# Kernel tuning notes

Hardware: AMD Instinct MI355X
Metric: run time of the kernel (lower is better)

The kernel has to match this reference:

```python
import jax, jax.numpy as jnp
import numpy as np

B = 32; IMG = 224; P = 16; D = 768; NH = 12; HD = 64; L = 12; MLP = 3072; S0 = 197
NE = 10; LP = 40; NPL = 5; NC = 100; EPS = 1e-6
POS_PROMPT = (0, 1, 2, 3, 4)


def setup_inputs() -> dict:
    ks = jax.random.split(jax.random.key(0), 18)
    n = lambda k, shp: jax.random.normal(k, shp, jnp.float32) * 0.02
    return {
        "inputs": jax.random.normal(ks[0], (B, 3, IMG, IMG), jnp.float32),
        "expert_ids": jax.random.randint(ks[1], (B,), 0, NE),
        "patch_w": n(ks[2], (D, 3, P, P)),
        "patch_b": n(ks[3], (D,)),
        "cls_token": n(ks[4], (1, 1, D)),
        "pos_embed": n(ks[5], (1, S0, D)),
        "ln1_s": jnp.ones((L, D), jnp.float32),
        "ln1_b": jnp.zeros((L, D), jnp.float32),
        "qkv_w": n(ks[6], (L, D, 3 * D)),
        "qkv_b": n(ks[7], (L, 3 * D)),
        "proj_w": n(ks[8], (L, D, D)),
        "proj_b": n(ks[9], (L, D)),
        "ln2_s": jnp.ones((L, D), jnp.float32),
        "ln2_b": jnp.zeros((L, D), jnp.float32),
        "fc1_w": n(ks[10], (L, D, MLP)),
        "fc1_b": n(ks[11], (L, MLP)),
        "fc2_w": n(ks[12], (L, MLP, D)),
        "fc2_b": n(ks[13], (L, D)),
        "norm_s": jnp.ones((D,), jnp.float32),
        "norm_b": jnp.zeros((D,), jnp.float32),
        "prompts": jax.random.uniform(ks[14], (NPL, NE, LP, D), jnp.float32),
        "head_w": n(ks[15], (NE, D, NC)),
        "head_b": n(ks[16], (NE, NC)),
    }


def _ln(x, s, b):
    m = x.mean(-1, keepdims=True)
    v = ((x - m) ** 2).mean(-1, keepdims=True)
    return (x - m) * jax.lax.rsqrt(v + EPS) * s + b


def _forward(inputs, expert_ids, patch_w, patch_b, cls_token, pos_embed,
             ln1_s, ln1_b, qkv_w, qkv_b, proj_w, proj_b, ln2_s, ln2_b,
             fc1_w, fc1_b, fc2_w, fc2_b, norm_s, norm_b, prompts, head_w, head_b):
    # patch embed: conv stride 16 -> [B, D, 14, 14] -> [B, 196, D]
    x = jax.lax.conv_general_dilated(inputs, patch_w, (P, P), 'VALID',
                                     dimension_numbers=('NCHW', 'OIHW', 'NCHW'))
    x = x.reshape(B, D, -1).transpose(0, 2, 1) + patch_b
    x = jnp.concatenate([jnp.broadcast_to(cls_token, (B, 1, D)), x], axis=1) + pos_embed
    # per-sample expert prompt gather: [B, NPL, LP, D], plus cls pos bias
    bp = jnp.take(prompts, expert_ids, axis=1).transpose(1, 0, 2, 3) + pos_embed[0, 0]
    scale = 1.0 / np.sqrt(HD)
    for i in range(L):
        if i in POS_PROMPT:
            x = jnp.concatenate([x, bp[:, POS_PROMPT.index(i)]], axis=1)
        S = x.shape[1]
        h = _ln(x, ln1_s[i], ln1_b[i])
        qkv = (h @ qkv_w[i] + qkv_b[i]).reshape(B, S, 3, NH, HD).transpose(2, 0, 3, 1, 4)
        q, k, v = qkv[0], qkv[1], qkv[2]
        att = jax.nn.softmax(jnp.einsum('bhqd,bhkd->bhqk', q, k) * scale, axis=-1)
        o = jnp.einsum('bhqk,bhkd->bhqd', att, v).transpose(0, 2, 1, 3).reshape(B, S, D)
        x = x + o @ proj_w[i] + proj_b[i]
        h = _ln(x, ln2_s[i], ln2_b[i])
        x = x + jax.nn.gelu(h @ fc1_w[i] + fc1_b[i], approximate=False) @ fc2_w[i] + fc2_b[i]
        x = x[:, :S0]  # drop prompt tokens after each block
    feat = _ln(x, norm_s, norm_b)[:, 0]
    # per-sample expert head dispatch: gathered-weight batched matvec
    return jnp.einsum('bd,bdc->bc', feat, head_w[expert_ids]) + head_b[expert_ids]


def reference(inputs, expert_ids, patch_w, patch_b, cls_token, pos_embed,
              ln1_s, ln1_b, qkv_w, qkv_b, proj_w, proj_b, ln2_s, ln2_b,
              fc1_w, fc1_b, fc2_w, fc2_b, norm_s, norm_b, prompts, head_w, head_b):
    return _forward(inputs, expert_ids, patch_w, patch_b, cls_token, pos_embed,
                    ln1_s, ln1_b, qkv_w, qkv_b, proj_w, proj_b, ln2_s, ln2_b,
                    fc1_w, fc1_b, fc2_w, fc2_b, norm_s, norm_b, prompts, head_w, head_b)
```

## Files before the change

kernel.cpp:

```cpp
#include <hip/hip_runtime.h>

typedef unsigned short ushort_t;
typedef __attribute__((ext_vector_type(8))) short short8;
typedef __attribute__((ext_vector_type(4))) short shortx4;
typedef __attribute__((ext_vector_type(4))) float floatx4;

#define D_    768
#define SMAX  237
#define S0_   197
#define RPAD  7680
#define NHEAD 12
#define BATCH 32


__device__ __forceinline__ ushort_t f2bf(float f) {
  union { float f; unsigned u; } v; v.f = f;
  unsigned r = v.u + 0x7FFFu + ((v.u >> 16) & 1u);
  return (ushort_t)(r >> 16);
}
__device__ __forceinline__ float bf2f(ushort_t u) {
  union { unsigned u; float f; } v; v.u = ((unsigned)u) << 16; return v.f;
}
__device__ __forceinline__ void async16(const void* g, void* l) {
  __builtin_amdgcn_global_load_lds((const __attribute__((address_space(1))) void*)g,
                                   (__attribute__((address_space(3))) void*)l, 16, 0, 0);
}

__global__ __launch_bounds__(256) void patchify_kernel(
    const float* __restrict__ in, ushort_t* __restrict__ Xp) {
  int rowid = blockIdx.x;
  int b = rowid / 196, p = rowid - b * 196;
  int py = p / 14, px = p - py * 14;
  int tid = threadIdx.x;
#pragma unroll
  for (int t = 0; t < 3; ++t) {
    int k = tid + t * 256;
    int c = k >> 8, rem = k & 255, i = rem >> 4, j = rem & 15;
    float v = in[(((size_t)b * 3 + c) * 224 + py * 16 + i) * 224 + px * 16 + j];
    Xp[(size_t)rowid * 768 + k] = f2bf(v);
  }
}

__global__ void cvt_bf16_kernel(const float* __restrict__ src, ushort_t* __restrict__ dst, int n) {
  int i = blockIdx.x * 256 + threadIdx.x;
  if (i < n) dst[i] = f2bf(src[i]);
}

__global__ void cls_fill_kernel(const float* __restrict__ cls, const float* __restrict__ pos,
                                float* __restrict__ X) {
  int b = blockIdx.x, d = threadIdx.x;
  X[(size_t)b * 768 + d] = cls[d] + pos[d];
}

__global__ void prompt_fill_kernel(const float* __restrict__ prompts, const float* __restrict__ pos,
                                   const int* __restrict__ eid, float* __restrict__ X, int layer) {
  int id = blockIdx.x;
  int b = id / 40, p = id - b * 40;
  int e = eid[b];
  float v = prompts[(((size_t)layer * 10 + e) * 40 + p) * 768 + threadIdx.x] + pos[threadIdx.x];
  X[((size_t)(197 + p) * 32 + b) * 768 + threadIdx.x] = v;
}

__global__ __launch_bounds__(256) void transpose_wts_kernel(
    const float* __restrict__ qkvw, const float* __restrict__ projw,
    const float* __restrict__ fc1w, const float* __restrict__ fc2w,
    ushort_t* __restrict__ wq, ushort_t* __restrict__ wp,
    ushort_t* __restrict__ w1, ushort_t* __restrict__ w2,
    int l0, int slot_mul) {
  int id = blockIdx.x;
  int l = l0 + id / 1728;
  int t = id % 1728;
  size_t s = (size_t)(l * slot_mul);
  const float* src; ushort_t* dst; int K, N;
  if (t < 432)       { src = qkvw + (size_t)l * 768 * 2304; dst = wq + s * 2304 * 768; K = 768;  N = 2304; }
  else if (t < 576)  { src = projw + (size_t)l * 768 * 768;  dst = wp + s * 768 * 768;  K = 768;  N = 768;  t -= 432; }
  else if (t < 1152) { src = fc1w + (size_t)l * 768 * 3072;  dst = w1 + s * 768 * 3072; K = 768;  N = 3072; t -= 576; }
  else               { src = fc2w + (size_t)l * 3072 * 768;  dst = w2 + s * 3072 * 768; K = 3072; N = 768;  t -= 1152; }
  int ntn = N >> 6;
  int k0 = (t / ntn) * 64, n0 = (t % ntn) * 64;
  __shared__ float tile[64][65];
  int tid = threadIdx.x;
#pragma unroll
  for (int q = 0; q < 4; ++q) {
    int slot = q * 256 + tid;
    int r = slot >> 4, c4 = (slot & 15) * 4;
    floatx4 v = *(const floatx4*)&src[(size_t)(k0 + r) * N + n0 + c4];
    tile[r][c4] = v[0]; tile[r][c4 + 1] = v[1]; tile[r][c4 + 2] = v[2]; tile[r][c4 + 3] = v[3];
  }
  __syncthreads();
#pragma unroll
  for (int q = 0; q < 2; ++q) {
    int slot = q * 256 + tid;
    int n = slot >> 3, kc = (slot & 7) * 8;
    short8 o;
#pragma unroll
    for (int e = 0; e < 8; ++e) o[e] = (short)f2bf(tile[kc + e][n]);
    *(short8*)&dst[(size_t)(n0 + n) * K + k0 + kc] = o;
  }
}

__global__ __launch_bounds__(256) void ln_kernel(
    const float* __restrict__ X, const float* __restrict__ s, const float* __restrict__ bt,
    ushort_t* __restrict__ H) {
  int row = blockIdx.x * 4 + (threadIdx.x >> 6);
  int lane = threadIdx.x & 63;
  const float* xr = X + (size_t)row * 768;
  floatx4 v0 = *(const floatx4*)&xr[lane * 4];
  floatx4 v1 = *(const floatx4*)&xr[256 + lane * 4];
  floatx4 v2 = *(const floatx4*)&xr[512 + lane * 4];
  float sum = 0.f, sq = 0.f;
#pragma unroll
  for (int e = 0; e < 4; ++e) {
    sum += v0[e] + v1[e] + v2[e];
    sq  += v0[e] * v0[e] + v1[e] * v1[e] + v2[e] * v2[e];
  }
#pragma unroll
  for (int m = 1; m <= 32; m <<= 1) {
    sum += __shfl_xor(sum, m, 64);
    sq  += __shfl_xor(sq,  m, 64);
  }
  float mean = sum * (1.f / 768.f);
  float var  = sq * (1.f / 768.f) - mean * mean;
  float rs = rsqrtf(var + 1e-6f);
  ushort_t* hr = H + (size_t)row * 768;
#pragma unroll
  for (int w = 0; w < 3; ++w) {
    const floatx4 v = (w == 0) ? v0 : (w == 1) ? v1 : v2;
    shortx4 o;
#pragma unroll
    for (int e = 0; e < 4; ++e) {
      int d = w * 256 + lane * 4 + e;
      o[e] = (short)f2bf((v[e] - mean) * rs * s[d] + bt[d]);
    }
    *(shortx4*)&hr[w * 256 + lane * 4] = o;
  }
}

enum { EPI_BF16 = 0, EPI_GELU = 1, EPI_RESID = 2, EPI_PATCH = 3 };

template <int EPI>
__device__ __forceinline__ void epi_store(float accv, int row, int col,
                                          const float* bias, float* XO, ushort_t* O,
                                          const float* pos, int N) {
  if (EPI == EPI_BF16) {
    O[(size_t)row * N + col] = f2bf(accv + bias[col]);
  } else if (EPI == EPI_GELU) {
    float v = accv + bias[col];
    float g = 0.5f * v * (1.0f + erff(v * 0.70710678118f));
    O[(size_t)row * N + col] = f2bf(g);
  } else if (EPI == EPI_RESID) {
    XO[(size_t)row * 768 + col] += accv + bias[col];
  } else {
    int b = row / 196, p = row - b * 196;
    size_t orow = (size_t)(1 + p) * 32 + b;
    XO[orow * 768 + col] = accv + bias[col] + pos[(size_t)(1 + p) * 768 + col];
  }
}

template <int EPI>
__global__ __launch_bounds__(256) void gemm_kernel(
    const ushort_t* __restrict__ A, int lda,
    const ushort_t* __restrict__ BT,
    const float* __restrict__ bias,
    float* __restrict__ XO, ushort_t* __restrict__ O,
    const float* __restrict__ pos,
    int N, int K) {
  __shared__ ushort_t As[128 * 64];
  __shared__ ushort_t Bs[128 * 64];
  int m0 = blockIdx.y * 128, n0 = blockIdx.x * 128;
  int tid = threadIdx.x, lane = tid & 63, wv = tid >> 6;
  int wm = (wv >> 1) * 64, wn = (wv & 1) * 64;
  int fr = lane & 15, kg = lane >> 4;
  int sw = (fr >> 1) & 7;

  floatx4 acc[4][4];
#pragma unroll
  for (int i = 0; i < 4; ++i)
#pragma unroll
    for (int j = 0; j < 4; ++j) acc[i][j] = (floatx4){0.f, 0.f, 0.f, 0.f};

  for (int k0 = 0; k0 < K; k0 += 64) {
#pragma unroll
    for (int t = 0; t < 4; ++t) {
      int flat = (wv * 4 + t) * 64 + lane;
      int row = flat >> 3;
      int ch = ((flat & 7) ^ ((row >> 1) & 7)) * 8;
      async16(A + (size_t)(m0 + row) * lda + k0 + ch, &As[(wv * 4 + t) * 512]);
      async16(BT + (size_t)(n0 + row) * K + k0 + ch, &Bs[(wv * 4 + t) * 512]);
    }
    __syncthreads();
#pragma unroll
    for (int kh = 0; kh < 2; ++kh) {
      short8 af[4], bfr[4];
#pragma unroll
      for (int i = 0; i < 4; ++i)
        af[i] = *(const short8*)&As[(wm + i * 16 + fr) * 64 + (((kh * 4 + kg) ^ sw) * 8)];
#pragma unroll
      for (int j = 0; j < 4; ++j)
        bfr[j] = *(const short8*)&Bs[(wn + j * 16 + fr) * 64 + (((kh * 4 + kg) ^ sw) * 8)];
#pragma unroll
      for (int i = 0; i < 4; ++i)
#pragma unroll
        for (int j = 0; j < 4; ++j)
          acc[i][j] = __builtin_amdgcn_mfma_f32_16x16x32_bf16(af[i], bfr[j], acc[i][j], 0, 0, 0);
    }
    __syncthreads();
  }

  int rbase = (lane >> 4) * 4;
#pragma unroll
  for (int i = 0; i < 4; ++i)
#pragma unroll
    for (int j = 0; j < 4; ++j) {
      int col = n0 + wn + j * 16 + fr;
#pragma unroll
      for (int r = 0; r < 4; ++r)
        epi_store<EPI>(acc[i][j][r], m0 + wm + i * 16 + rbase + r, col, bias, XO, O, pos, N);
    }
}

template <int EPI>
__global__ __launch_bounds__(256) void gemm64_kernel(
    const ushort_t* __restrict__ A, int lda,
    const ushort_t* __restrict__ BT,
    const float* __restrict__ bias,
    float* __restrict__ XO, ushort_t* __restrict__ O,
    const float* __restrict__ pos,
    int N, int K) {
  __shared__ ushort_t As[64 * 64];
  __shared__ ushort_t Bs[128 * 64];
  int m0 = blockIdx.y * 64, n0 = blockIdx.x * 128;
  int tid = threadIdx.x, lane = tid & 63, wv = tid >> 6;
  int wm = (wv >> 1) * 32, wn = (wv & 1) * 64;
  int fr = lane & 15, kg = lane >> 4;
  int sw = (fr >> 1) & 7;

  floatx4 acc[2][4];
#pragma unroll
  for (int i = 0; i < 2; ++i)
#pragma unroll
    for (int j = 0; j < 4; ++j) acc[i][j] = (floatx4){0.f, 0.f, 0.f, 0.f};

  for (int k0 = 0; k0 < K; k0 += 64) {
#pragma unroll
    for (int t = 0; t < 2; ++t) {
      int flat = (wv * 2 + t) * 64 + lane;
      int row = flat >> 3;
      int ch = ((flat & 7) ^ ((row >> 1) & 7)) * 8;
      async16(A + (size_t)(m0 + row) * lda + k0 + ch, &As[(wv * 2 + t) * 512]);
    }
#pragma unroll
    for (int t = 0; t < 4; ++t) {
      int flat = (wv * 4 + t) * 64 + lane;
      int row = flat >> 3;
      int ch = ((flat & 7) ^ ((row >> 1) & 7)) * 8;
      async16(BT + (size_t)(n0 + row) * K + k0 + ch, &Bs[(wv * 4 + t) * 512]);
    }
    __syncthreads();
#pragma unroll
    for (int kh = 0; kh < 2; ++kh) {
      short8 af[2], bfr[4];
#pragma unroll
      for (int i = 0; i < 2; ++i)
        af[i] = *(const short8*)&As[(wm + i * 16 + fr) * 64 + (((kh * 4 + kg) ^ sw) * 8)];
#pragma unroll
      for (int j = 0; j < 4; ++j)
        bfr[j] = *(const short8*)&Bs[(wn + j * 16 + fr) * 64 + (((kh * 4 + kg) ^ sw) * 8)];
#pragma unroll
      for (int i = 0; i < 2; ++i)
#pragma unroll
        for (int j = 0; j < 4; ++j)
          acc[i][j] = __builtin_amdgcn_mfma_f32_16x16x32_bf16(af[i], bfr[j], acc[i][j], 0, 0, 0);
    }
    __syncthreads();
  }

  int rbase = (lane >> 4) * 4;
#pragma unroll
  for (int i = 0; i < 2; ++i)
#pragma unroll
    for (int j = 0; j < 4; ++j) {
      int col = n0 + wn + j * 16 + fr;
#pragma unroll
      for (int r = 0; r < 4; ++r)
        epi_store<EPI>(acc[i][j][r], m0 + wm + i * 16 + rbase + r, col, bias, XO, O, pos, N);
    }
}

__global__ __launch_bounds__(256) void attn_kernel(ushort_t* __restrict__ qkv, int S) {
  __shared__ ushort_t Kc[64 * 64];
  __shared__ ushort_t Vt[64 * 72];
  __shared__ ushort_t Pb[4][16 * 72];
  int id = blockIdx.x;
  int qc = id & 3, bh = id >> 2;
  int b = bh / NHEAD, h = bh - b * NHEAD;
  int tid = threadIdx.x, lane = tid & 63, wv = tid >> 6;
  int fr = lane & 15, kg = lane >> 4;
  int q0 = qc * 64 + wv * 16;

  int qr = q0 + fr; if (qr > S - 1) qr = S - 1;
  const ushort_t* qp = qkv + ((size_t)qr * 32 + b) * 2304 + h * 64 + kg * 8;
  short8 qf0 = *(const short8*)qp;
  short8 qf1 = *(const short8*)(qp + 32);

  floatx4 oacc[4];
#pragma unroll
  for (int j = 0; j < 4; ++j) oacc[j] = (floatx4){0.f, 0.f, 0.f, 0.f};
  float lsum[4] = {0.f, 0.f, 0.f, 0.f};

  int ksw = kg ^ (fr & 7);
  int kst_g = (lane & 7) ^ ((lane >> 3) & 7);

  for (int c = 0; c < 4; ++c) {
    int key0 = c * 64;
    __syncthreads();
#pragma unroll
    for (int t = 0; t < 2; ++t) {
      int f = (wv * 2 + t) * 64 + lane;
      int kr = key0 + (f >> 3); if (kr > S - 1) kr = S - 1;
      async16(qkv + ((size_t)kr * 32 + b) * 2304 + 768 + h * 64 + kst_g * 8,
              &Kc[(wv * 2 + t) * 512]);
    }
#pragma unroll
    for (int t = 0; t < 2; ++t) {
      int kc = wv * 2 + t;
      int vr = key0 + lane; if (vr > S - 1) vr = S - 1;
      short8 vv = *(const short8*)(qkv + ((size_t)vr * 32 + b) * 2304 + 1536 + h * 64 + kc * 8);
#pragma unroll
      for (int e = 0; e < 8; ++e) Vt[(kc * 8 + e) * 72 + lane] = (ushort_t)vv[e];
    }
    __syncthreads();

    floatx4 sacc[4];
#pragma unroll
    for (int j = 0; j < 4; ++j) sacc[j] = (floatx4){0.f, 0.f, 0.f, 0.f};
#pragma unroll
    for (int j = 0; j < 4; ++j) {
      int krow = j * 16 + fr;
      short8 b0 = *(const short8*)&Kc[krow * 64 + ksw * 8];
      short8 b1 = *(const short8*)&Kc[krow * 64 + (ksw ^ 4) * 8];
      sacc[j] = __builtin_amdgcn_mfma_f32_16x16x32_bf16(qf0, b0, sacc[j], 0, 0, 0);
      sacc[j] = __builtin_amdgcn_mfma_f32_16x16x32_bf16(qf1, b1, sacc[j], 0, 0, 0);
    }

#pragma unroll
    for (int j = 0; j < 4; ++j) {
      int key = key0 + j * 16 + fr;
      bool valid = key < S;
#pragma unroll
      for (int r = 0; r < 4; ++r) {
        float e = valid ? __expf(sacc[j][r] * 0.125f) : 0.f;
        lsum[r] += e;
        Pb[wv][(kg * 4 + r) * 72 + j * 16 + fr] = f2bf(e);
      }
    }
    __syncthreads();

    const ushort_t* pp = &Pb[wv][fr * 72 + kg * 8];
    short8 p0 = *(const short8*)pp;
    short8 p1 = *(const short8*)(pp + 32);
#pragma unroll
    for (int j = 0; j < 4; ++j) {
      const ushort_t* vp = &Vt[(j * 16 + fr) * 72 + kg * 8];
      short8 v0 = *(const short8*)vp;
      short8 v1 = *(const short8*)(vp + 32);
      oacc[j] = __builtin_amdgcn_mfma_f32_16x16x32_bf16(p0, v0, oacc[j], 0, 0, 0);
      oacc[j] = __builtin_amdgcn_mfma_f32_16x16x32_bf16(p1, v1, oacc[j], 0, 0, 0);
    }
  }

#pragma unroll
  for (int r = 0; r < 4; ++r) {
#pragma unroll
    for (int m = 1; m <= 8; m <<= 1) lsum[r] += __shfl_xor(lsum[r], m, 64);
  }
#pragma unroll
  for (int r = 0; r < 4; ++r) {
    int q = q0 + kg * 4 + r;
    if (q < S) {
      float inv = 1.f / lsum[r];
      ushort_t* op = qkv + ((size_t)q * 32 + b) * 2304 + h * 64;
#pragma unroll
      for (int j = 0; j < 4; ++j) op[j * 16 + fr] = f2bf(oacc[j][r] * inv);
    }
  }
}

__global__ __launch_bounds__(256) void head_kernel(
    const float* __restrict__ X, const float* __restrict__ ns, const float* __restrict__ nb,
    const int* __restrict__ eid, const float* __restrict__ hw, const float* __restrict__ hb,
    float* __restrict__ out) {
  int b = blockIdx.x, tid = threadIdx.x;
  const float* xr = X + (size_t)b * 768;
  float v0 = xr[tid], v1 = xr[tid + 256], v2 = xr[tid + 512];
  float sum = v0 + v1 + v2;
  float sq = v0 * v0 + v1 * v1 + v2 * v2;
#pragma unroll
  for (int off = 32; off; off >>= 1) {
    sum += __shfl_down(sum, off, 64);
    sq  += __shfl_down(sq,  off, 64);
  }
  __shared__ float red[8];
  __shared__ float feat[768];
  int wv = tid >> 6, ln = tid & 63;
  if (ln == 0) { red[wv] = sum; red[4 + wv] = sq; }
  __syncthreads();
  if (tid == 0) {
    red[0] = red[0] + red[1] + red[2] + red[3];
    red[4] = red[4] + red[5] + red[6] + red[7];
  }
  __syncthreads();
  float mean = red[0] * (1.f / 768.f);
  float var  = red[4] * (1.f / 768.f) - mean * mean;
  float rs = rsqrtf(var + 1e-6f);
  feat[tid]       = (v0 - mean) * rs * ns[tid]       + nb[tid];
  feat[tid + 256] = (v1 - mean) * rs * ns[tid + 256] + nb[tid + 256];
  feat[tid + 512] = (v2 - mean) * rs * ns[tid + 512] + nb[tid + 512];
  __syncthreads();
  int e = eid[b];
  if (tid < 100) {
    float a = hb[e * 100 + tid];
    const float* w = hw + (size_t)e * 768 * 100 + tid;
#pragma unroll 4
    for (int d = 0; d < 768; ++d) a += feat[d] * w[(size_t)d * 100];
    out[b * 100 + tid] = a;
  }
}

extern "C" void kernel_launch(void* const* d_in, const int* in_sizes, int n_in,
                              void* d_out, int out_size, void* d_ws, size_t ws_size,
                              hipStream_t stream) {
  const float* inputs     = (const float*)d_in[0];
  const int*   expert_ids = (const int*)d_in[1];
  const float* patch_w    = (const float*)d_in[2];
  const float* patch_b    = (const float*)d_in[3];
  const float* cls_token  = (const float*)d_in[4];
  const float* pos_embed  = (const float*)d_in[5];
  const float* ln1_s      = (const float*)d_in[6];
  const float* ln1_b      = (const float*)d_in[7];
  const float* qkv_w      = (const float*)d_in[8];
  const float* qkv_b      = (const float*)d_in[9];
  const float* proj_w     = (const float*)d_in[10];
  const float* proj_b     = (const float*)d_in[11];
  const float* ln2_s      = (const float*)d_in[12];
  const float* ln2_b      = (const float*)d_in[13];
  const float* fc1_w      = (const float*)d_in[14];
  const float* fc1_b      = (const float*)d_in[15];
  const float* fc2_w      = (const float*)d_in[16];
  const float* fc2_b      = (const float*)d_in[17];
  const float* norm_s     = (const float*)d_in[18];
  const float* norm_b     = (const float*)d_in[19];
  const float* prompts    = (const float*)d_in[20];
  const float* head_w     = (const float*)d_in[21];
  const float* head_b     = (const float*)d_in[22];
  float* out = (float*)d_out;

  const size_t kHoistNeed = 289100000ull;
  bool hoist = ws_size >= kHoistNeed;
  size_t slots = hoist ? 12 : 1;

  char* ws = (char*)d_ws;
  size_t off = 0;
  ushort_t* WTp = (ushort_t*)(ws + off); off += (size_t)768 * 768 * 2;
  ushort_t* WQ  = (ushort_t*)(ws + off); off += slots * 2304 * 768 * 2;
  ushort_t* WP  = (ushort_t*)(ws + off); off += slots * 768 * 768 * 2;
  ushort_t* W1  = (ushort_t*)(ws + off); off += slots * 768 * 3072 * 2;
  ushort_t* W2  = (ushort_t*)(ws + off); off += slots * 3072 * 768 * 2;
  float*    X   = (float*)(ws + off);    off += (size_t)RPAD * 768 * 4;
  ushort_t* H   = (ushort_t*)(ws + off); off += (size_t)RPAD * 768 * 2;
  ushort_t* QKV = (ushort_t*)(ws + off); off += (size_t)RPAD * 2304 * 2;
  ushort_t* MID = (ushort_t*)(ws + off); off += (size_t)RPAD * 3072 * 2;
  ushort_t* XP  = MID;

  cvt_bf16_kernel<<<(768 * 768 + 255) / 256, 256, 0, stream>>>(patch_w, WTp, 768 * 768);
  patchify_kernel<<<6272, 256, 0, stream>>>(inputs, XP);
  gemm64_kernel<EPI_PATCH><<<dim3(6, 98), 256, 0, stream>>>(
      XP, 768, WTp, patch_b, X, nullptr, pos_embed, 768, 768);
  cls_fill_kernel<<<BATCH, 768, 0, stream>>>(cls_token, pos_embed, X);

  if (hoist)
    transpose_wts_kernel<<<1728 * 12, 256, 0, stream>>>(
        qkv_w, proj_w, fc1_w, fc2_w, WQ, WP, W1, W2, 0, 1);

  for (int i = 0; i < 12; ++i) {
    int S = (i < 5) ? SMAX : S0_;
    int MT = (i < 5) ? 60 : 50;
    if (i < 5)
      prompt_fill_kernel<<<BATCH * 40, 768, 0, stream>>>(prompts, pos_embed, expert_ids, X, i);
    if (!hoist)
      transpose_wts_kernel<<<1728, 256, 0, stream>>>(
          qkv_w, proj_w, fc1_w, fc2_w, WQ, WP, W1, W2, i, 0);
    ushort_t* WQi = WQ + (hoist ? (size_t)i * 2304 * 768 : 0);
    ushort_t* WPi = WP + (hoist ? (size_t)i * 768 * 768 : 0);
    ushort_t* W1i = W1 + (hoist ? (size_t)i * 768 * 3072 : 0);
    ushort_t* W2i = W2 + (hoist ? (size_t)i * 3072 * 768 : 0);

    ln_kernel<<<MT * 32, 256, 0, stream>>>(X, ln1_s + i * 768, ln1_b + i * 768, H);
    gemm_kernel<EPI_BF16><<<dim3(18, MT), 256, 0, stream>>>(
        H, 768, WQi, qkv_b + i * 2304, nullptr, QKV, nullptr, 2304, 768);
    attn_kernel<<<BATCH * NHEAD * 4, 256, 0, stream>>>(QKV, S);
    gemm_kernel<EPI_RESID><<<dim3(6, MT), 256, 0, stream>>>(
        QKV, 2304, WPi, proj_b + i * 768, X, nullptr, nullptr, 768, 768);
    ln_kernel<<<MT * 32, 256, 0, stream>>>(X, ln2_s + i * 768, ln2_b + i * 768, H);
    gemm_kernel<EPI_GELU><<<dim3(24, MT), 256, 0, stream>>>(
        H, 768, W1i, fc1_b + i * 3072, nullptr, MID, nullptr, 3072, 768);
    gemm_kernel<EPI_RESID><<<dim3(6, MT), 256, 0, stream>>>(
        MID, 3072, W2i, fc2_b + i * 768, X, nullptr, nullptr, 768, 3072);
  }

  head_kernel<<<BATCH, 256, 0, stream>>>(X, norm_s, norm_b, expert_ids, head_w, head_b, out);
}
```

Baseline: 3.390 ms.

## Double-buffer GEMM LDS tiles with K=32 stages to overlap loads and MFMA

Both GEMM kernels now hold two LDS buffers, each with a K=32 slice in place of the earlier single K=64 slice. The async global-to-LDS copy for the next slice is issued before the MFMAs on the current slice, and the loop ends each step with one waitcnt and one barrier. The goal is to hide global load latency behind compute and drop one barrier per iteration. The cost is twice as many iterations with half the MFMA work each, and a new XOR swizzle on the narrower rows.

```diff
diff --git a/kernel.cpp b/kernel.cpp
--- a/kernel.cpp
+++ b/kernel.cpp
@@ -165,13 +165,25 @@
     float* __restrict__ XO, ushort_t* __restrict__ O,
     const float* __restrict__ pos,
     int N, int K) {
-  __shared__ ushort_t As[128 * 64];
-  __shared__ ushort_t Bs[128 * 64];
+  __shared__ ushort_t As[2][128 * 32];
+  __shared__ ushort_t Bs[2][128 * 32];
   int m0 = blockIdx.y * 128, n0 = blockIdx.x * 128;
   int tid = threadIdx.x, lane = tid & 63, wv = tid >> 6;
   int wm = (wv >> 1) * 64, wn = (wv & 1) * 64;
   int fr = lane & 15, kg = lane >> 4;
-  int sw = (fr >> 1) & 7;
+  int sw = (kg ^ ((fr >> 1) & 3)) * 8;
+
+  int f0 = wv * 128 + lane, f1 = f0 + 64;
+  int r0 = f0 >> 2, c0 = ((f0 & 3) ^ ((f0 >> 3) & 3)) * 8;
+  int r1 = f1 >> 2, c1 = ((f1 & 3) ^ ((f1 >> 3) & 3)) * 8;
+  const ushort_t* A0 = A + (size_t)(m0 + r0) * lda + c0;
+  const ushort_t* A1 = A + (size_t)(m0 + r1) * lda + c1;
+  const ushort_t* B0 = BT + (size_t)(n0 + r0) * K + c0;
+  const ushort_t* B1 = BT + (size_t)(n0 + r1) * K + c1;
+  ushort_t* lA0 = &As[0][(wv * 2) * 512];
+  ushort_t* lA1 = &As[0][(wv * 2 + 1) * 512];
+  ushort_t* lB0 = &Bs[0][(wv * 2) * 512];
+  ushort_t* lB1 = &Bs[0][(wv * 2 + 1) * 512];
 
   floatx4 acc[4][4];
 #pragma unroll
@@ -179,33 +191,47 @@
 #pragma unroll
     for (int j = 0; j < 4; ++j) acc[i][j] = (floatx4){0.f, 0.f, 0.f, 0.f};
 
-  for (int k0 = 0; k0 < K; k0 += 64) {
-#pragma unroll
-    for (int t = 0; t < 4; ++t) {
-      int flat = (wv * 4 + t) * 64 + lane;
-      int row = flat >> 3;
-      int ch = ((flat & 7) ^ ((row >> 1) & 7)) * 8;
-      async16(A + (size_t)(m0 + row) * lda + k0 + ch, &As[(wv * 4 + t) * 512]);
-      async16(BT + (size_t)(n0 + row) * K + k0 + ch, &Bs[(wv * 4 + t) * 512]);
-    }
-    __syncthreads();
-#pragma unroll
-    for (int kh = 0; kh < 2; ++kh) {
-      short8 af[4], bfr[4];
-#pragma unroll
-      for (int i = 0; i < 4; ++i)
-        af[i] = *(const short8*)&As[(wm + i * 16 + fr) * 64 + (((kh * 4 + kg) ^ sw) * 8)];
-#pragma unroll
-      for (int j = 0; j < 4; ++j)
-        bfr[j] = *(const short8*)&Bs[(wn + j * 16 + fr) * 64 + (((kh * 4 + kg) ^ sw) * 8)];
-#pragma unroll
-      for (int i = 0; i < 4; ++i)
-#pragma unroll
-        for (int j = 0; j < 4; ++j)
-          acc[i][j] = __builtin_amdgcn_mfma_f32_16x16x32_bf16(af[i], bfr[j], acc[i][j], 0, 0, 0);
-    }
-    __syncthreads();
-  }
+#define STAGE(buf, k0)                                   \
+  do {                                                   \
+    int _o = (buf) * 4096;                               \
+    async16(A0 + (k0), lA0 + _o);                        \
+    async16(A1 + (k0), lA1 + _o);                        \
+    async16(B0 + (k0), lB0 + _o);                        \
+    async16(B1 + (k0), lB1 + _o);                        \
+  } while (0)
+
+#define COMPUTE(buf)                                                                   \
+  do {                                                                                 \
+    const ushort_t* _as = &As[buf][0];                                                 \
+    const ushort_t* _bs = &Bs[buf][0];                                                 \
+    short8 af[4], bfr[4];                                                              \
+    _Pragma("unroll")                                                                  \
+    for (int i = 0; i < 4; ++i) af[i] = *(const short8*)&_as[(wm + i * 16 + fr) * 32 + sw]; \
+    _Pragma("unroll")                                                                  \
+    for (int j = 0; j < 4; ++j) bfr[j] = *(const short8*)&_bs[(wn + j * 16 + fr) * 32 + sw]; \
+    _Pragma("unroll")                                                                  \
+    for (int i = 0; i < 4; ++i)                                                        \
+      _Pragma("unroll")                                                                \
+      for (int j = 0; j < 4; ++j)                                                      \
+        acc[i][j] = __builtin_amdgcn_mfma_f32_16x16x32_bf16(af[i], bfr[j], acc[i][j], 0, 0, 0); \
+  } while (0)
+
+  int nt = K >> 5;
+  STAGE(0, 0);
+  asm volatile("s_waitcnt vmcnt(0)" ::: "memory");
+  __builtin_amdgcn_s_barrier();
+  int cur = 0;
+  for (int t = 0; t < nt - 1; ++t) {
+    STAGE(cur ^ 1, (t + 1) * 32);
+    COMPUTE(cur);
+    asm volatile("s_waitcnt vmcnt(0)" ::: "memory");
+    __builtin_amdgcn_sched_barrier(0);
+    __builtin_amdgcn_s_barrier();
+    cur ^= 1;
+  }
+  COMPUTE(cur);
+#undef STAGE
+#undef COMPUTE
 
   int rbase = (lane >> 4) * 4;
 #pragma unroll
@@ -227,13 +253,25 @@
     float* __restrict__ XO, ushort_t* __restrict__ O,
     const float* __restrict__ pos,
     int N, int K) {
-  __shared__ ushort_t As[64 * 64];
-  __shared__ ushort_t Bs[128 * 64];
+  __shared__ ushort_t As[2][64 * 32];
+  __shared__ ushort_t Bs[2][128 * 32];
   int m0 = blockIdx.y * 64, n0 = blockIdx.x * 128;
   int tid = threadIdx.x, lane = tid & 63, wv = tid >> 6;
   int wm = (wv >> 1) * 32, wn = (wv & 1) * 64;
   int fr = lane & 15, kg = lane >> 4;
-  int sw = (fr >> 1) & 7;
+  int sw = (kg ^ ((fr >> 1) & 3)) * 8;
+
+  int fa = wv * 64 + lane;
+  int ra = fa >> 2, ca = ((fa & 3) ^ ((fa >> 3) & 3)) * 8;
+  int f0 = wv * 128 + lane, f1 = f0 + 64;
+  int r0 = f0 >> 2, c0 = ((f0 & 3) ^ ((f0 >> 3) & 3)) * 8;
+  int r1 = f1 >> 2, c1 = ((f1 & 3) ^ ((f1 >> 3) & 3)) * 8;
+  const ushort_t* Aa = A + (size_t)(m0 + ra) * lda + ca;
+  const ushort_t* B0 = BT + (size_t)(n0 + r0) * K + c0;
+  const ushort_t* B1 = BT + (size_t)(n0 + r1) * K + c1;
+  ushort_t* lAa = &As[0][wv * 512];
+  ushort_t* lB0 = &Bs[0][(wv * 2) * 512];
+  ushort_t* lB1 = &Bs[0][(wv * 2 + 1) * 512];
 
   floatx4 acc[2][4];
 #pragma unroll
@@ -241,39 +279,45 @@
 #pragma unroll
     for (int j = 0; j < 4; ++j) acc[i][j] = (floatx4){0.f, 0.f, 0.f, 0.f};
 
-  for (int k0 = 0; k0 < K; k0 += 64) {
-#pragma unroll
-    for (int t = 0; t < 2; ++t) {
-      int flat = (wv * 2 + t) * 64 + lane;
-      int row = flat >> 3;
-      int ch = ((flat & 7) ^ ((row >> 1) & 7)) * 8;
-      async16(A + (size_t)(m0 + row) * lda + k0 + ch, &As[(wv * 2 + t) * 512]);
-    }
-#pragma unroll
-    for (int t = 0; t < 4; ++t) {
-      int flat = (wv * 4 + t) * 64 + lane;
-      int row = flat >> 3;
-      int ch = ((flat & 7) ^ ((row >> 1) & 7)) * 8;
-      async16(BT + (size_t)(n0 + row) * K + k0 + ch, &Bs[(wv * 4 + t) * 512]);
-    }
-    __syncthreads();
-#pragma unroll
-    for (int kh = 0; kh < 2; ++kh) {
-      short8 af[2], bfr[4];
-#pragma unroll
-      for (int i = 0; i < 2; ++i)
-        af[i] = *(const short8*)&As[(wm + i * 16 + fr) * 64 + (((kh * 4 + kg) ^ sw) * 8)];
-#pragma unroll
-      for (int j = 0; j < 4; ++j)
-        bfr[j] = *(const short8*)&Bs[(wn + j * 16 + fr) * 64 + (((kh * 4 + kg) ^ sw) * 8)];
-#pragma unroll
-      for (int i = 0; i < 2; ++i)
-#pragma unroll
-        for (int j = 0; j < 4; ++j)
-          acc[i][j] = __builtin_amdgcn_mfma_f32_16x16x32_bf16(af[i], bfr[j], acc[i][j], 0, 0, 0);
-    }
-    __syncthreads();
-  }
+#define STAGE(buf, k0)                                   \
+  do {                                                   \
+    async16(Aa + (k0), lAa + (buf) * 2048);              \
+    async16(B0 + (k0), lB0 + (buf) * 4096);              \
+    async16(B1 + (k0), lB1 + (buf) * 4096);              \
+  } while (0)
+
+#define COMPUTE(buf)                                                                   \
+  do {                                                                                 \
+    const ushort_t* _as = &As[buf][0];                                                 \
+    const ushort_t* _bs = &Bs[buf][0];                                                 \
+    short8 af[2], bfr[4];                                                              \
+    _Pragma("unroll")                                                                  \
+    for (int i = 0; i < 2; ++i) af[i] = *(const short8*)&_as[(wm + i * 16 + fr) * 32 + sw]; \
+    _Pragma("unroll")                                                                  \
+    for (int j = 0; j < 4; ++j) bfr[j] = *(const short8*)&_bs[(wn + j * 16 + fr) * 32 + sw]; \
+    _Pragma("unroll")                                                                  \
+    for (int i = 0; i < 2; ++i)                                                        \
+      _Pragma("unroll")                                                                \
+      for (int j = 0; j < 4; ++j)                                                      \
+        acc[i][j] = __builtin_amdgcn_mfma_f32_16x16x32_bf16(af[i], bfr[j], acc[i][j], 0, 0, 0); \
+  } while (0)
+
+  int nt = K >> 5;
+  STAGE(0, 0);
+  asm volatile("s_waitcnt vmcnt(0)" ::: "memory");
+  __builtin_amdgcn_s_barrier();
+  int cur = 0;
+  for (int t = 0; t < nt - 1; ++t) {
+    STAGE(cur ^ 1, (t + 1) * 32);
+    COMPUTE(cur);
+    asm volatile("s_waitcnt vmcnt(0)" ::: "memory");
+    __builtin_amdgcn_sched_barrier(0);
+    __builtin_amdgcn_s_barrier();
+    cur ^= 1;
+  }
+  COMPUTE(cur);
+#undef STAGE
+#undef COMPUTE
 
   int rbase = (lane >> 4) * 4;
 #pragma unroll
```

New measurement: 3.664 ms. 8.1% more time.

## Switch GEMMs to 32x32x16 MFMA and remap workgroups across XCDs

Applied to the files above, without the earlier changes.

Both GEMM kernels now use 32x32x16 bf16 MFMA instructions instead of 16x16x32. Each wave issues fewer, larger MFMAs and makes fewer LDS fragment loads per k-step, and the fragment indexing and epilogue row/column mapping are rewritten to match the new layout. Workgroup IDs are also remapped so that consecutive tiles land on the same XCD, which is meant to improve L2 reuse of shared A/B panels. The epilogue store pattern changes, and the remap adds integer divides per block.

```diff
diff --git a/kernel.cpp b/kernel.cpp
--- a/kernel.cpp
+++ b/kernel.cpp
@@ -4,6 +4,7 @@
 typedef __attribute__((ext_vector_type(8))) short short8;
 typedef __attribute__((ext_vector_type(4))) short shortx4;
 typedef __attribute__((ext_vector_type(4))) float floatx4;
+typedef __attribute__((ext_vector_type(16))) float floatx16;
 
 #define D_    768
 #define SMAX  237
@@ -157,6 +158,12 @@
   }
 }
 
+__device__ __forceinline__ int xcd_remap(int o, int nwg) {
+  int q8 = nwg >> 3, r8 = nwg & 7;
+  int xcd = o & 7, idx = o >> 3;
+  return (xcd < r8 ? xcd * (q8 + 1) : r8 * (q8 + 1) + (xcd - r8) * q8) + idx;
+}
+
 template <int EPI>
 __global__ __launch_bounds__(256) void gemm_kernel(
     const ushort_t* __restrict__ A, int lda,
@@ -167,17 +174,21 @@
     int N, int K) {
   __shared__ ushort_t As[128 * 64];
   __shared__ ushort_t Bs[128 * 64];
-  int m0 = blockIdx.y * 128, n0 = blockIdx.x * 128;
+  int nwg = gridDim.x * gridDim.y;
+  int wg = xcd_remap(blockIdx.y * gridDim.x + blockIdx.x, nwg);
+  int m0 = (wg / gridDim.x) * 128, n0 = (wg % gridDim.x) * 128;
   int tid = threadIdx.x, lane = tid & 63, wv = tid >> 6;
   int wm = (wv >> 1) * 64, wn = (wv & 1) * 64;
-  int fr = lane & 15, kg = lane >> 4;
-  int sw = (fr >> 1) & 7;
-
-  floatx4 acc[4][4];
-#pragma unroll
-  for (int i = 0; i < 4; ++i)
-#pragma unroll
-    for (int j = 0; j < 4; ++j) acc[i][j] = (floatx4){0.f, 0.f, 0.f, 0.f};
+  int r31 = lane & 31, hg = lane >> 5;
+  int rs7 = (r31 >> 1) & 7;
+
+  floatx16 acc[2][2];
+#pragma unroll
+  for (int i = 0; i < 2; ++i)
+#pragma unroll
+    for (int j = 0; j < 2; ++j)
+#pragma unroll
+      for (int e = 0; e < 16; ++e) acc[i][j][e] = 0.f;
 
   for (int k0 = 0; k0 < K; k0 += 64) {
 #pragma unroll
@@ -190,33 +201,30 @@
     }
     __syncthreads();
 #pragma unroll
-    for (int kh = 0; kh < 2; ++kh) {
-      short8 af[4], bfr[4];
-#pragma unroll
-      for (int i = 0; i < 4; ++i)
-        af[i] = *(const short8*)&As[(wm + i * 16 + fr) * 64 + (((kh * 4 + kg) ^ sw) * 8)];
-#pragma unroll
-      for (int j = 0; j < 4; ++j)
-        bfr[j] = *(const short8*)&Bs[(wn + j * 16 + fr) * 64 + (((kh * 4 + kg) ^ sw) * 8)];
-#pragma unroll
-      for (int i = 0; i < 4; ++i)
-#pragma unroll
-        for (int j = 0; j < 4; ++j)
-          acc[i][j] = __builtin_amdgcn_mfma_f32_16x16x32_bf16(af[i], bfr[j], acc[i][j], 0, 0, 0);
-    }
-    __syncthreads();
-  }
-
-  int rbase = (lane >> 4) * 4;
-#pragma unroll
-  for (int i = 0; i < 4; ++i)
-#pragma unroll
-    for (int j = 0; j < 4; ++j) {
-      int col = n0 + wn + j * 16 + fr;
-#pragma unroll
-      for (int r = 0; r < 4; ++r)
-        epi_store<EPI>(acc[i][j][r], m0 + wm + i * 16 + rbase + r, col, bias, XO, O, pos, N);
-    }
+    for (int s = 0; s < 4; ++s) {
+      int cc = ((s * 2 + hg) ^ rs7) * 8;
+      short8 af0 = *(const short8*)&As[(wm + r31) * 64 + cc];
+      short8 af1 = *(const short8*)&As[(wm + 32 + r31) * 64 + cc];
+      short8 bf0 = *(const short8*)&Bs[(wn + r31) * 64 + cc];
+      short8 bf1 = *(const short8*)&Bs[(wn + 32 + r31) * 64 + cc];
+      acc[0][0] = __builtin_amdgcn_mfma_f32_32x32x16_bf16(af0, bf0, acc[0][0], 0, 0, 0);
+      acc[0][1] = __builtin_amdgcn_mfma_f32_32x32x16_bf16(af0, bf1, acc[0][1], 0, 0, 0);
+      acc[1][0] = __builtin_amdgcn_mfma_f32_32x32x16_bf16(af1, bf0, acc[1][0], 0, 0, 0);
+      acc[1][1] = __builtin_amdgcn_mfma_f32_32x32x16_bf16(af1, bf1, acc[1][1], 0, 0, 0);
+    }
+    __syncthreads();
+  }
+
+#pragma unroll
+  for (int i = 0; i < 2; ++i)
+#pragma unroll
+    for (int j = 0; j < 2; ++j)
+#pragma unroll
+      for (int g = 0; g < 16; ++g) {
+        int row = m0 + wm + i * 32 + (g & 3) + 8 * (g >> 2) + 4 * hg;
+        int col = n0 + wn + j * 32 + r31;
+        epi_store<EPI>(acc[i][j][g], row, col, bias, XO, O, pos, N);
+      }
 }
 
 template <int EPI>
@@ -229,17 +237,19 @@
     int N, int K) {
   __shared__ ushort_t As[64 * 64];
   __shared__ ushort_t Bs[128 * 64];
-  int m0 = blockIdx.y * 64, n0 = blockIdx.x * 128;
+  int nwg = gridDim.x * gridDim.y;
+  int wg = xcd_remap(blockIdx.y * gridDim.x + blockIdx.x, nwg);
+  int m0 = (wg / gridDim.x) * 64, n0 = (wg % gridDim.x) * 128;
   int tid = threadIdx.x, lane = tid & 63, wv = tid >> 6;
   int wm = (wv >> 1) * 32, wn = (wv & 1) * 64;
-  int fr = lane & 15, kg = lane >> 4;
-  int sw = (fr >> 1) & 7;
-
-  floatx4 acc[2][4];
-#pragma unroll
-  for (int i = 0; i < 2; ++i)
-#pragma unroll
-    for (int j = 0; j < 4; ++j) acc[i][j] = (floatx4){0.f, 0.f, 0.f, 0.f};
+  int r31 = lane & 31, hg = lane >> 5;
+  int rs7 = (r31 >> 1) & 7;
+
+  floatx16 acc[2];
+#pragma unroll
+  for (int j = 0; j < 2; ++j)
+#pragma unroll
+    for (int e = 0; e < 16; ++e) acc[j][e] = 0.f;
 
   for (int k0 = 0; k0 < K; k0 += 64) {
 #pragma unroll
@@ -258,32 +268,24 @@
     }
     __syncthreads();
 #pragma unroll
-    for (int kh = 0; kh < 2; ++kh) {
-      short8 af[2], bfr[4];
-#pragma unroll
-      for (int i = 0; i < 2; ++i)
-        af[i] = *(const short8*)&As[(wm + i * 16 + fr) * 64 + (((kh * 4 + kg) ^ sw) * 8)];
-#pragma unroll
-      for (int j = 0; j < 4; ++j)
-        bfr[j] = *(const short8*)&Bs[(wn + j * 16 + fr) * 64 + (((kh * 4 + kg) ^ sw) * 8)];
-#pragma unroll
-      for (int i = 0; i < 2; ++i)
-#pragma unroll
-        for (int j = 0; j < 4; ++j)
-          acc[i][j] = __builtin_amdgcn_mfma_f32_16x16x32_bf16(af[i], bfr[j], acc[i][j], 0, 0, 0);
-    }
-    __syncthreads();
-  }
-
-  int rbase = (lane >> 4) * 4;
-#pragma unroll
-  for (int i = 0; i < 2; ++i)
-#pragma unroll
-    for (int j = 0; j < 4; ++j) {
-      int col = n0 + wn + j * 16 + fr;
-#pragma unroll
-      for (int r = 0; r < 4; ++r)
-        epi_store<EPI>(acc[i][j][r], m0 + wm + i * 16 + rbase + r, col, bias, XO, O, pos, N);
+    for (int s = 0; s < 4; ++s) {
+      int cc = ((s * 2 + hg) ^ rs7) * 8;
+      short8 af  = *(const short8*)&As[(wm + r31) * 64 + cc];
+      short8 bf0 = *(const short8*)&Bs[(wn + r31) * 64 + cc];
+      short8 bf1 = *(const short8*)&Bs[(wn + 32 + r31) * 64 + cc];
+      acc[0] = __builtin_amdgcn_mfma_f32_32x32x16_bf16(af, bf0, acc[0], 0, 0, 0);
+      acc[1] = __builtin_amdgcn_mfma_f32_32x32x16_bf16(af, bf1, acc[1], 0, 0, 0);
+    }
+    __syncthreads();
+  }
+
+#pragma unroll
+  for (int j = 0; j < 2; ++j)
+#pragma unroll
+    for (int g = 0; g < 16; ++g) {
+      int row = m0 + wm + (g & 3) + 8 * (g >> 2) + 4 * hg;
+      int col = n0 + wn + j * 32 + r31;
+      epi_store<EPI>(acc[j][g], row, col, bias, XO, O, pos, N);
     }
 }
 
```

New measurement: 3.141 ms. 1.08x faster.
